# Performance work log

Measured on AMD Instinct MI355X. Metric: run time of the kernel, lower is better.

Reference implementation:

```python
import jax, jax.numpy as jnp
import numpy as np

B, I, N = 512, 128, 256
ODE_UNFOLDS = 6

def setup_inputs() -> dict:
    key = jax.random.key(0)
    ks = jax.random.split(key, 16)
    u = lambda k, shape, lo, hi: jax.random.uniform(k, shape, jnp.float32, lo, hi)
    inputs = jax.random.normal(ks[0], (B, I), jnp.float32)
    state = jax.random.normal(ks[1], (B, N), jnp.float32)
    sensory_mu = u(ks[2], (I, N), 0.3, 0.8)
    sensory_sigma = u(ks[3], (I, N), 3.0, 8.0)
    sensory_W = u(ks[4], (I, N), 0.01, 1.0)
    sensory_erev = (2.0 * jax.random.randint(ks[5], (I, N), 0, 2).astype(jnp.float32) - 1.0)
    mu = u(ks[6], (N, N), 0.3, 0.8)
    sigma = u(ks[7], (N, N), 3.0, 8.0)
    W = u(ks[8], (N, N), 0.01, 1.0)
    erev = (2.0 * jax.random.randint(ks[9], (N, N), 0, 2).astype(jnp.float32) - 1.0)
    vleak = u(ks[10], (N,), -0.2, 0.2)
    gleak = jnp.ones((N,), jnp.float32)         # gleak_init_min == gleak_init_max == 1.0
    cm_t = jnp.full((N,), 0.5, jnp.float32)     # cm_init_min == cm_init_max == 0.5
    return dict(inputs=inputs, state=state, sensory_mu=sensory_mu,
                sensory_sigma=sensory_sigma, sensory_W=sensory_W,
                sensory_erev=sensory_erev, mu=mu, sigma=sigma, W=W, erev=erev,
                vleak=vleak, gleak=gleak, cm_t=cm_t)

def reference(inputs, state, sensory_mu, sensory_sigma, sensory_W, sensory_erev,
              mu, sigma, W, erev, vleak, gleak, cm_t):
    # sensory gating: (B, I, N)
    s_act = sensory_W * jax.nn.sigmoid(sensory_sigma * (inputs[:, :, None] - sensory_mu))
    w_num_sensory = jnp.sum(s_act * sensory_erev, axis=1)  # (B, N)
    w_den_sensory = jnp.sum(s_act, axis=1)                 # (B, N)

    def step(v_pre, _):
        # recurrent gating: (B, N, N)
        w_act = W * jax.nn.sigmoid(sigma * (v_pre[:, :, None] - mu))
        w_num = jnp.sum(w_act * erev, axis=1) + w_num_sensory
        w_den = jnp.sum(w_act, axis=1) + w_den_sensory
        numerator = cm_t * v_pre + gleak * vleak + w_num
        denominator = cm_t + gleak + w_den
        return numerator / denominator, None

    v, _ = jax.lax.scan(step, state, None, length=ODE_UNFOLDS)
    return (v, v)
```

## Files before the change

kernel.cpp:

```cpp
#include <hip/hip_runtime.h>
#include <stdint.h>

#define NN 256
#define II 128
#define BATCH 512
#define STEPS 6
#define LOG2E 1.4426950408889634f

typedef _Float16 half_t;
typedef _Float16 h2 __attribute__((ext_vector_type(2)));
typedef float v2f __attribute__((ext_vector_type(2)));

__global__ void pack_f16(const float* __restrict__ sigma, const float* __restrict__ mu,
                         const float* __restrict__ W, const float* __restrict__ erev,
                         uint4* __restrict__ pq4, uint2* __restrict__ w2, int ni)
{
    int gid = blockIdx.x * blockDim.x + threadIdx.x;
    int total = (ni / 16) * 1024;
    if (gid >= total) return;
    int ip2 = gid >> 10, t = gid & 1023;
    int q = t & 3, j = t >> 2;
    int i0 = q * (ni / 4) + ip2 * 4;
    unsigned pw[4];
    half_t wa[4];
    #pragma unroll
    for (int e = 0; e < 4; ++e) {
        int k = (i0 + e) * NN + j;
        float sg = sigma[k];
        h2 pq = { (half_t)(-LOG2E * sg), (half_t)(LOG2E * sg * mu[k]) };
        pw[e] = __builtin_bit_cast(unsigned, pq);
        wa[e] = (half_t)(W[k] * erev[k]);
    }
    pq4[gid] = make_uint4(pw[0], pw[1], pw[2], pw[3]);
    h2 w01 = { wa[0], wa[1] }, w23 = { wa[2], wa[3] };
    w2[gid] = make_uint2(__builtin_bit_cast(unsigned, w01),
                         __builtin_bit_cast(unsigned, w23));
}

__device__ __forceinline__ void proc_pair(unsigned pq0, unsigned pq1, unsigned wp,
                                          float va, float vb, v2f& an, v2f& ad)
{
    h2 P0 = __builtin_bit_cast(h2, pq0);
    h2 P1 = __builtin_bit_cast(h2, pq1);
    h2 Wh = __builtin_bit_cast(h2, wp);
    float e0 = __builtin_amdgcn_exp2f(fmaf((float)P0.x, va, (float)P0.y));
    float e1 = __builtin_amdgcn_exp2f(fmaf((float)P1.x, vb, (float)P1.y));
    float b0 = e0 + 1.f, b1 = e1 + 1.f;
    float rr = __builtin_amdgcn_rcpf(b0 * b1);
    float t0 = fmaf((float)Wh.x, b1, 0.0f);
    float t1 = fmaf((float)Wh.y, b0, 0.0f);
    an.x = fmaf(t0, rr, an.x);
    ad.x = fmaf(fabsf(t0), rr, ad.x);
    an.y = fmaf(t1, rr, an.y);
    ad.y = fmaf(fabsf(t1), rr, ad.y);
}

__global__ __launch_bounds__(1024, 8)
void ltc_f16(const float* __restrict__ inputs, const float* __restrict__ state,
             const uint4* __restrict__ spq, const uint2* __restrict__ sw,
             const uint4* __restrict__ rpq, const uint2* __restrict__ rw,
             const float* __restrict__ vleak, const float* __restrict__ gleak,
             const float* __restrict__ cm, float* __restrict__ out)
{
    __shared__ __align__(16) float v_sh[2][4][NN + 4];
    __shared__ __align__(16) float x_sh[4][II + 4];

    const int tid = threadIdx.x;
    const int q   = tid & 3;
    const int j   = tid >> 2;
    const int row = blockIdx.x;

    if (tid < II) {
        float xv = inputs[row * II + tid];
        #pragma unroll
        for (int c = 0; c < 4; ++c) x_sh[c][tid] = xv;
    } else if (tid >= 512 && tid < 512 + NN) {
        float vv = state[row * NN + (tid - 512)];
        #pragma unroll
        for (int c = 0; c < 4; ++c) v_sh[0][c][tid - 512] = vv;
    }
    const float c    = cm[j];
    const float g    = gleak[j];
    const float glvl = g * vleak[j];
    const float denb = c + g;
    __syncthreads();

    float sn, sd;
    {
        v2f an = {0.f, 0.f}, ad = {0.f, 0.f};
        const uint4* pp = spq + tid;
        const uint2* pw = sw + tid;
        #pragma unroll
        for (int ip2 = 0; ip2 < 8; ++ip2, pp += 1024, pw += 1024) {
            uint4 u = *pp;
            uint2 w = *pw;
            float4 xv = *(const float4*)&x_sh[q][q * 32 + ip2 * 4];
            proc_pair(u.x, u.y, w.x, xv.x, xv.y, an, ad);
            proc_pair(u.z, u.w, w.y, xv.z, xv.w, an, ad);
        }
        sn = an.x + an.y;
        sd = ad.x + ad.y;
        sn += __shfl_xor(sn, 1, 64); sn += __shfl_xor(sn, 2, 64);
        sd += __shfl_xor(sd, 1, 64); sd += __shfl_xor(sd, 2, 64);
    }

    int cur = 0;
    for (int step = 0; step < STEPS; ++step) {
        v2f an = {0.f, 0.f}, ad = {0.f, 0.f};
        const uint4* pp = rpq + tid;
        const uint2* pw = rw + tid;
        #pragma unroll 4
        for (int ip2 = 0; ip2 < 16; ++ip2, pp += 1024, pw += 1024) {
            uint4 u = *pp;
            uint2 w = *pw;
            float4 vv = *(const float4*)&v_sh[cur][q][q * 64 + ip2 * 4];
            proc_pair(u.x, u.y, w.x, vv.x, vv.y, an, ad);
            proc_pair(u.z, u.w, w.y, vv.z, vv.w, an, ad);
        }
        float rn = an.x + an.y;
        float rd = ad.x + ad.y;
        rn += __shfl_xor(rn, 1, 64); rn += __shfl_xor(rn, 2, 64);
        rd += __shfl_xor(rd, 1, 64); rd += __shfl_xor(rd, 2, 64);

        float wn = rn + sn, wd = rd + sd;
        float vp = v_sh[cur][q][j];
        float vn = (fmaf(c, vp, glvl) + wn) * __builtin_amdgcn_rcpf(denb + wd);
        v_sh[cur ^ 1][q][j] = vn;
        if (q == 0 && step == STEPS - 1) {
            out[row * NN + j] = vn;
            out[BATCH * NN + row * NN + j] = vn;
        }
        __syncthreads();
        cur ^= 1;
    }
}

__global__ __launch_bounds__(1024, 4)
void ltc_fallback(const float* __restrict__ inputs, const float* __restrict__ state,
                  const float* __restrict__ s_sigma, const float* __restrict__ s_mu,
                  const float* __restrict__ s_W, const float* __restrict__ s_erev,
                  const float* __restrict__ r_sigma, const float* __restrict__ r_mu,
                  const float* __restrict__ r_W, const float* __restrict__ r_erev,
                  const float* __restrict__ vleak, const float* __restrict__ gleak,
                  const float* __restrict__ cm, float* __restrict__ out)
{
    __shared__ float  v_sh[2][NN];
    __shared__ float  x_sh[2][II];
    __shared__ float2 sens_sh[2][NN];
    __shared__ float2 part[8][NN];

    const int tid  = threadIdx.x;
    const int j    = tid & (NN - 1);
    const int q    = tid >> 8;
    const int row0 = blockIdx.x * 2;

    if (tid < 2 * NN) {
        int r = tid >> 8, cc = tid & (NN - 1);
        v_sh[r][cc] = state[(row0 + r) * NN + cc];
    } else if (tid < 2 * NN + 2 * II) {
        int t = tid - 2 * NN;
        x_sh[t >> 7][t & (II - 1)] = inputs[(row0 + (t >> 7)) * II + (t & (II - 1))];
    }

    const int r2 = tid >> 8;
    float cmv = 0.f, glvl = 0.f, denb = 0.f;
    if (tid < 512) {
        float cc = cm[j], gg = gleak[j];
        cmv = cc; glvl = gg * vleak[j]; denb = cc + gg;
    }
    __syncthreads();

    {
        float sn[2] = {0.f, 0.f}, sd[2] = {0.f, 0.f};
        for (int ii = 0; ii < 32; ++ii) {
            const int i = q * 32 + ii;
            int k = i * NN + j;
            float sg = s_sigma[k];
            float p = -LOG2E * sg, qq = LOG2E * sg * s_mu[k];
            float w = s_W[k] * s_erev[k];
            #pragma unroll
            for (int r = 0; r < 2; ++r) {
                float e = __builtin_amdgcn_exp2f(fmaf(p, x_sh[r][i], qq));
                float t = w * __builtin_amdgcn_rcpf(1.f + e);
                sn[r] += t; sd[r] += fabsf(t);
            }
        }
        part[q * 2 + 0][j] = make_float2(sn[0], sd[0]);
        part[q * 2 + 1][j] = make_float2(sn[1], sd[1]);
    }
    __syncthreads();
    if (tid < 512) {
        float2 a0 = part[0 + r2][j], a1 = part[2 + r2][j], a2 = part[4 + r2][j], a3 = part[6 + r2][j];
        sens_sh[r2][j] = make_float2(a0.x + a1.x + a2.x + a3.x, a0.y + a1.y + a2.y + a3.y);
    }
    __syncthreads();

    for (int step = 0; step < STEPS; ++step) {
        float sn[2] = {0.f, 0.f}, sd[2] = {0.f, 0.f};
        for (int ii = 0; ii < 64; ++ii) {
            const int i = q * 64 + ii;
            int k = i * NN + j;
            float sg = r_sigma[k];
            float p = -LOG2E * sg, qq = LOG2E * sg * r_mu[k];
            float w = r_W[k] * r_erev[k];
            #pragma unroll
            for (int r = 0; r < 2; ++r) {
                float e = __builtin_amdgcn_exp2f(fmaf(p, v_sh[r][i], qq));
                float t = w * __builtin_amdgcn_rcpf(1.f + e);
                sn[r] += t; sd[r] += fabsf(t);
            }
        }
        part[q * 2 + 0][j] = make_float2(sn[0], sd[0]);
        part[q * 2 + 1][j] = make_float2(sn[1], sd[1]);
        __syncthreads();

        if (tid < 512) {
            float2 a0 = part[0 + r2][j], a1 = part[2 + r2][j], a2 = part[4 + r2][j], a3 = part[6 + r2][j];
            float wn = a0.x + a1.x + a2.x + a3.x + sens_sh[r2][j].x;
            float wd = a0.y + a1.y + a2.y + a3.y + sens_sh[r2][j].y;
            float vp = v_sh[r2][j];
            float vn = (fmaf(cmv, vp, glvl) + wn) * __builtin_amdgcn_rcpf(denb + wd);
            v_sh[r2][j] = vn;
            if (step == STEPS - 1) {
                out[(row0 + r2) * NN + j] = vn;
                out[BATCH * NN + (row0 + r2) * NN + j] = vn;
            }
        }
        __syncthreads();
    }
}

extern "C" void kernel_launch(void* const* d_in, const int* in_sizes, int n_in,
                              void* d_out, int out_size, void* d_ws, size_t ws_size,
                              hipStream_t stream)
{
    const float* inputs  = (const float*)d_in[0];
    const float* state   = (const float*)d_in[1];
    const float* s_mu    = (const float*)d_in[2];
    const float* s_sigma = (const float*)d_in[3];
    const float* s_W     = (const float*)d_in[4];
    const float* s_erev  = (const float*)d_in[5];
    const float* mu      = (const float*)d_in[6];
    const float* sigma   = (const float*)d_in[7];
    const float* W       = (const float*)d_in[8];
    const float* erev    = (const float*)d_in[9];
    const float* vleak   = (const float*)d_in[10];
    const float* gleak   = (const float*)d_in[11];
    const float* cm      = (const float*)d_in[12];
    float* out = (float*)d_out;

    const size_t need = 16384 * 16 + 16384 * 8 + 8192 * 16 + 8192 * 8;
    if (ws_size >= need) {
        char* p = (char*)d_ws;
        uint4* rpq = (uint4*)p;
        uint2* rw  = (uint2*)(p + 16384 * 16);
        uint4* spq = (uint4*)(p + 16384 * 16 + 16384 * 8);
        uint2* sw  = (uint2*)(p + 16384 * 16 + 16384 * 8 + 8192 * 16);
        pack_f16<<<64, 256, 0, stream>>>(sigma, mu, W, erev, rpq, rw, NN);
        pack_f16<<<32, 256, 0, stream>>>(s_sigma, s_mu, s_W, s_erev, spq, sw, II);
        ltc_f16<<<BATCH, 1024, 0, stream>>>(inputs, state, spq, sw, rpq, rw,
                                            vleak, gleak, cm, out);
    } else {
        ltc_fallback<<<BATCH / 2, 1024, 0, stream>>>(
            inputs, state, s_sigma, s_mu, s_W, s_erev, sigma, mu, W, erev,
            vleak, gleak, cm, out);
    }
}
```

Baseline: 78.21 us.

## Compute sigmoid gating in packed fp16 with polynomial exp2 and shared reciprocal

Replaces the per-element fp32 hardware exp2 with a packed-half exp2 built from a clamp, a magic-number round, a cubic polynomial and an exponent bit-shift. Four denominators now share one reciprocal instead of one per pair. The packed layout is changed to separate slope and offset pairs, and shared-memory state and inputs are held as fp16. This is meant to cut transcendental and VALU instruction count, at the cost of accuracy: the state is rounded to half every step, and clamping the exponent to [-14,15] may distort saturated sigmoids.

```diff
diff --git a/kernel.cpp b/kernel.cpp
--- a/kernel.cpp
+++ b/kernel.cpp
@@ -9,7 +9,10 @@
 
 typedef _Float16 half_t;
 typedef _Float16 h2 __attribute__((ext_vector_type(2)));
+typedef unsigned short us2 __attribute__((ext_vector_type(2)));
 typedef float v2f __attribute__((ext_vector_type(2)));
+
+__device__ __forceinline__ h2 bch2(unsigned u) { return __builtin_bit_cast(h2, u); }
 
 __global__ void pack_f16(const float* __restrict__ sigma, const float* __restrict__ mu,
                          const float* __restrict__ W, const float* __restrict__ erev,
@@ -21,38 +24,80 @@
     int ip2 = gid >> 10, t = gid & 1023;
     int q = t & 3, j = t >> 2;
     int i0 = q * (ni / 4) + ip2 * 4;
-    unsigned pw[4];
-    half_t wa[4];
+    half_t p[4], qq[4], w[4];
     #pragma unroll
     for (int e = 0; e < 4; ++e) {
         int k = (i0 + e) * NN + j;
         float sg = sigma[k];
-        h2 pq = { (half_t)(-LOG2E * sg), (half_t)(LOG2E * sg * mu[k]) };
-        pw[e] = __builtin_bit_cast(unsigned, pq);
-        wa[e] = (half_t)(W[k] * erev[k]);
-    }
-    pq4[gid] = make_uint4(pw[0], pw[1], pw[2], pw[3]);
-    h2 w01 = { wa[0], wa[1] }, w23 = { wa[2], wa[3] };
-    w2[gid] = make_uint2(__builtin_bit_cast(unsigned, w01),
-                         __builtin_bit_cast(unsigned, w23));
-}
-
-__device__ __forceinline__ void proc_pair(unsigned pq0, unsigned pq1, unsigned wp,
-                                          float va, float vb, v2f& an, v2f& ad)
-{
-    h2 P0 = __builtin_bit_cast(h2, pq0);
-    h2 P1 = __builtin_bit_cast(h2, pq1);
-    h2 Wh = __builtin_bit_cast(h2, wp);
-    float e0 = __builtin_amdgcn_exp2f(fmaf((float)P0.x, va, (float)P0.y));
-    float e1 = __builtin_amdgcn_exp2f(fmaf((float)P1.x, vb, (float)P1.y));
-    float b0 = e0 + 1.f, b1 = e1 + 1.f;
-    float rr = __builtin_amdgcn_rcpf(b0 * b1);
-    float t0 = fmaf((float)Wh.x, b1, 0.0f);
-    float t1 = fmaf((float)Wh.y, b0, 0.0f);
-    an.x = fmaf(t0, rr, an.x);
-    ad.x = fmaf(fabsf(t0), rr, ad.x);
-    an.y = fmaf(t1, rr, an.y);
-    ad.y = fmaf(fabsf(t1), rr, ad.y);
+        p[e]  = (half_t)(-LOG2E * sg);
+        qq[e] = (half_t)(LOG2E * sg * mu[k]);
+        w[e]  = (half_t)(W[k] * erev[k]);
+    }
+    h2 p01 = {p[0], p[1]},  p23 = {p[2], p[3]};
+    h2 q01 = {qq[0], qq[1]}, q23 = {qq[2], qq[3]};
+    h2 w01 = {w[0], w[1]},  w23 = {w[2], w[3]};
+    pq4[gid] = make_uint4(__builtin_bit_cast(unsigned, p01), __builtin_bit_cast(unsigned, q01),
+                          __builtin_bit_cast(unsigned, p23), __builtin_bit_cast(unsigned, q23));
+    w2[gid]  = make_uint2(__builtin_bit_cast(unsigned, w01), __builtin_bit_cast(unsigned, w23));
+}
+
+__device__ __forceinline__ void proc_quad(uint4 u, uint2 wp, unsigned vv01, unsigned vv23,
+                                          v2f& an, v2f& ad)
+{
+    const h2 CHI = {(half_t)15.0f,   (half_t)15.0f};
+    const h2 CLO = {(half_t)-14.0f,  (half_t)-14.0f};
+    const h2 MAG = {(half_t)1536.0f, (half_t)1536.0f};
+    const h2 C3  = {(half_t)0.0558073f, (half_t)0.0558073f};
+    const h2 C2  = {(half_t)0.2401910f, (half_t)0.2401910f};
+    const h2 C1  = {(half_t)0.6931474f, (half_t)0.6931474f};
+    const h2 C0  = {(half_t)0.9999925f, (half_t)0.9999925f};
+    const h2 ONE = {(half_t)1.0f, (half_t)1.0f};
+    const us2 EBIAS = {0x3C00, 0x3C00};
+
+    h2 P01 = bch2(u.x), Q01 = bch2(u.y), P23 = bch2(u.z), Q23 = bch2(u.w);
+    h2 W01 = bch2(wp.x), W23 = bch2(wp.y);
+    h2 V01 = bch2(vv01), V23 = bch2(vv23);
+
+    h2 a01 = __builtin_elementwise_fma(P01, V01, Q01);
+    h2 a23 = __builtin_elementwise_fma(P23, V23, Q23);
+    a01 = __builtin_elementwise_max(__builtin_elementwise_min(a01, CHI), CLO);
+    a23 = __builtin_elementwise_max(__builtin_elementwise_min(a23, CHI), CLO);
+
+    h2 y01 = a01 + MAG,  y23 = a23 + MAG;
+    h2 n01 = y01 - MAG,  n23 = y23 - MAG;
+    h2 f01 = a01 - n01,  f23 = a23 - n23;
+
+    h2 r01 = __builtin_elementwise_fma(C3, f01, C2);
+    h2 r23 = __builtin_elementwise_fma(C3, f23, C2);
+    r01 = __builtin_elementwise_fma(r01, f01, C1);
+    r23 = __builtin_elementwise_fma(r23, f23, C1);
+    r01 = __builtin_elementwise_fma(r01, f01, C0);
+    r23 = __builtin_elementwise_fma(r23, f23, C0);
+
+    us2 s01 = (us2)(__builtin_bit_cast(us2, y01) << 10) + EBIAS;
+    us2 s23 = (us2)(__builtin_bit_cast(us2, y23) << 10) + EBIAS;
+
+    h2 b01 = __builtin_elementwise_fma(r01, __builtin_bit_cast(h2, s01), ONE);
+    h2 b23 = __builtin_elementwise_fma(r23, __builtin_bit_cast(h2, s23), ONE);
+
+    h2 t01 = W01 * __builtin_shufflevector(b01, b01, 1, 0);
+    h2 t23 = W23 * __builtin_shufflevector(b23, b23, 1, 0);
+
+    float b0 = (float)b01.x, b1 = (float)b01.y;
+    float b2 = (float)b23.x, b3 = (float)b23.y;
+    float p01f = b0 * b1, p23f = b2 * b3;
+    float r4 = __builtin_amdgcn_rcpf(p01f * p23f);
+    float rr01 = r4 * p23f;
+    float rr23 = r4 * p01f;
+
+    an.x = fmaf((float)t01.x, rr01, an.x);
+    an.y = fmaf((float)t01.y, rr01, an.y);
+    ad.x = fmaf(fabsf((float)t01.x), rr01, ad.x);
+    ad.y = fmaf(fabsf((float)t01.y), rr01, ad.y);
+    an.x = fmaf((float)t23.x, rr23, an.x);
+    an.y = fmaf((float)t23.y, rr23, an.y);
+    ad.x = fmaf(fabsf((float)t23.x), rr23, ad.x);
+    ad.y = fmaf(fabsf((float)t23.y), rr23, ad.y);
 }
 
 __global__ __launch_bounds__(1024, 8)
@@ -62,8 +107,8 @@
              const float* __restrict__ vleak, const float* __restrict__ gleak,
              const float* __restrict__ cm, float* __restrict__ out)
 {
-    __shared__ __align__(16) float v_sh[2][4][NN + 4];
-    __shared__ __align__(16) float x_sh[4][II + 4];
+    __shared__ __align__(16) half_t v_h[2][4][264];
+    __shared__ __align__(16) half_t x_h[4][136];
 
     const int tid = threadIdx.x;
     const int q   = tid & 3;
@@ -71,13 +116,13 @@
     const int row = blockIdx.x;
 
     if (tid < II) {
-        float xv = inputs[row * II + tid];
+        half_t xh = (half_t)inputs[row * II + tid];
         #pragma unroll
-        for (int c = 0; c < 4; ++c) x_sh[c][tid] = xv;
+        for (int c = 0; c < 4; ++c) x_h[c][tid] = xh;
     } else if (tid >= 512 && tid < 512 + NN) {
-        float vv = state[row * NN + (tid - 512)];
+        half_t vh = (half_t)state[row * NN + (tid - 512)];
         #pragma unroll
-        for (int c = 0; c < 4; ++c) v_sh[0][c][tid - 512] = vv;
+        for (int c = 0; c < 4; ++c) v_h[0][c][tid - 512] = vh;
     }
     const float c    = cm[j];
     const float g    = gleak[j];
@@ -90,13 +135,12 @@
         v2f an = {0.f, 0.f}, ad = {0.f, 0.f};
         const uint4* pp = spq + tid;
         const uint2* pw = sw + tid;
-        #pragma unroll
+        #pragma unroll 2
         for (int ip2 = 0; ip2 < 8; ++ip2, pp += 1024, pw += 1024) {
             uint4 u = *pp;
             uint2 w = *pw;
-            float4 xv = *(const float4*)&x_sh[q][q * 32 + ip2 * 4];
-            proc_pair(u.x, u.y, w.x, xv.x, xv.y, an, ad);
-            proc_pair(u.z, u.w, w.y, xv.z, xv.w, an, ad);
+            uint2 xv = *(const uint2*)&x_h[q][q * 32 + ip2 * 4];
+            proc_quad(u, w, xv.x, xv.y, an, ad);
         }
         sn = an.x + an.y;
         sd = ad.x + ad.y;
@@ -109,13 +153,12 @@
         v2f an = {0.f, 0.f}, ad = {0.f, 0.f};
         const uint4* pp = rpq + tid;
         const uint2* pw = rw + tid;
-        #pragma unroll 4
+        #pragma unroll 2
         for (int ip2 = 0; ip2 < 16; ++ip2, pp += 1024, pw += 1024) {
             uint4 u = *pp;
             uint2 w = *pw;
-            float4 vv = *(const float4*)&v_sh[cur][q][q * 64 + ip2 * 4];
-            proc_pair(u.x, u.y, w.x, vv.x, vv.y, an, ad);
-            proc_pair(u.z, u.w, w.y, vv.z, vv.w, an, ad);
+            uint2 vv = *(const uint2*)&v_h[cur][q][q * 64 + ip2 * 4];
+            proc_quad(u, w, vv.x, vv.y, an, ad);
         }
         float rn = an.x + an.y;
         float rd = ad.x + ad.y;
@@ -123,9 +166,9 @@
         rd += __shfl_xor(rd, 1, 64); rd += __shfl_xor(rd, 2, 64);
 
         float wn = rn + sn, wd = rd + sd;
-        float vp = v_sh[cur][q][j];
+        float vp = (float)v_h[cur][q][j];
         float vn = (fmaf(c, vp, glvl) + wn) * __builtin_amdgcn_rcpf(denb + wd);
-        v_sh[cur ^ 1][q][j] = vn;
+        v_h[cur ^ 1][q][j] = (half_t)vn;
         if (q == 0 && step == STEPS - 1) {
             out[row * NN + j] = vn;
             out[BATCH * NN + row * NN + j] = vn;
```

Result: slower. 95.68 us (+22.3%).
